# Kernel optimization log

Hardware: AMD Instinct MI355X
Metric: run time of the kernel (lower is better)

Reference implementation:

```python
import jax, jax.numpy as jnp
import numpy as np

EPS = 1e-5

def _ln(x, g, b):
    m = x.mean(-1, keepdims=True)
    v = ((x - m) ** 2).mean(-1, keepdims=True)
    return (x - m) / jnp.sqrt(v + EPS) * g + b


def setup_inputs() -> dict:
    key = jax.random.key(0)
    ks = jax.random.split(key, 8)
    b, t, n, d = 8, 12, 207, 64
    dh = 4 * d
    sc = 1.0 / np.sqrt(d)
    x = jax.random.normal(ks[0], (b, t, n, d), jnp.float32)
    stg = jax.random.uniform(ks[1], (b, t, n, t, n), jnp.float32)
    return {
        "x": x,
        "stg": stg,
        "Wq": jax.random.normal(ks[2], (d, d), jnp.float32) * sc,
        "bq": jnp.zeros((d,), jnp.float32),
        "Wk": jax.random.normal(ks[3], (d, d), jnp.float32) * sc,
        "bk": jnp.zeros((d,), jnp.float32),
        "gamma": jnp.ones((d,), jnp.float32),
        "beta": jnp.zeros((d,), jnp.float32),
        "fgamma": jnp.ones((d,), jnp.float32),
        "fbeta": jnp.zeros((d,), jnp.float32),
        "w1": jax.random.normal(ks[4], (d, dh), jnp.float32) * sc,
        "b1": jnp.zeros((dh,), jnp.float32),
        "w2": jax.random.normal(ks[5], (dh, d), jnp.float32) * (1.0 / np.sqrt(dh)),
        "b2": jnp.zeros((d,), jnp.float32),
        "topk": 3,
    }


def reference(x, stg, Wq, bq, Wk, bk, gamma, beta, fgamma, fbeta, w1, b1, w2, b2, topk):
    b, t, n, d = x.shape
    scale = 1.0 / np.sqrt(d).astype(np.float32)
    x_ = _ln(x, gamma, beta)
    y_ = x_  # trg is None path
    h = t
    q = y_ @ Wq + bq  # [b,t,n,d]
    kx = x_ @ Wk + bk  # [b,t,n,d]
    dg = jnp.einsum('btnd,bkmd->btnkm', q, kx) * scale  # [b,t,n,t,n]
    s = jax.nn.sigmoid(dg) * stg
    s = s.reshape(b, h * n, t * n)
    k_eff = topk * n if topk < 5 else topk  # torch: self.topk *= n when < 5
    top_vals = jax.lax.top_k(s, k_eff)[0]  # [b, h*n, k_eff]
    thr = top_vals[..., -1:]
    s = jnp.where(s > thr, s, -jnp.inf)
    a = jax.nn.softmax(s, axis=-1).reshape(b, h, n, t, n)  # dropout = identity (eval)
    o = jnp.einsum('btnkm,bkmd->btnd', a, x_)
    z = o + y_
    # FFN (assumed pre-norm residual MLP): x + relu(LN(x)W1+b1)W2 + b2
    hdd = jax.nn.relu(_ln(z, fgamma, fbeta) @ w1 + b1)
    return z + hdd @ w2 + b2
```

## Files before the change

### kernel.cpp

```cpp
#include <hip/hip_runtime.h>

#define NBATCH 8
#define NN     207
#define DHID   256
#define LL     2484
#define LLP    2496
#define RT     26
#define NBLK   96
#define GCOL   2560
#define TILES  78
#define TPW    10
#define SENT   0xFFFFu
#define LNEPS  1e-5f

typedef __attribute__((ext_vector_type(8)))  short bf16x8;
typedef __attribute__((ext_vector_type(8)))  unsigned short u16x8;
typedef __attribute__((ext_vector_type(16))) float f32x16;

__device__ __forceinline__ short f2bf(float f) {
    unsigned u = __float_as_uint(f);
    unsigned r = (u + 0x7FFFu + ((u >> 16) & 1u)) >> 16;
    return (short)r;
}

__global__ __launch_bounds__(256) void k_lnproj(
    const float* __restrict__ x, const float* __restrict__ Wq, const float* __restrict__ bq,
    const float* __restrict__ Wk, const float* __restrict__ bk,
    const float* __restrict__ gamma, const float* __restrict__ beta,
    float* __restrict__ Xn, float* __restrict__ Qb, short* __restrict__ Kbf)
{
    __shared__ float xrow[4][64];
    int w = threadIdx.x >> 6, lane = threadIdx.x & 63;
    size_t row = (size_t)blockIdx.x * 4 + w;
    float xv = x[row * 64 + lane];
    float m = xv;
    #pragma unroll
    for (int o = 32; o; o >>= 1) m += __shfl_xor(m, o, 64);
    m *= (1.0f / 64.0f);
    float dv = xv - m;
    float var = dv * dv;
    #pragma unroll
    for (int o = 32; o; o >>= 1) var += __shfl_xor(var, o, 64);
    var *= (1.0f / 64.0f);
    float xg = dv * (1.0f / sqrtf(var + LNEPS)) * gamma[lane] + beta[lane];
    Xn[row * 64 + lane] = xg;
    xrow[w][lane] = xg;
    __syncthreads();
    float q = bq[lane], k = bk[lane];
    #pragma unroll 8
    for (int e = 0; e < 64; e++) {
        float xe = xrow[w][e];
        q += xe * Wq[e * 64 + lane];
        k += xe * Wk[e * 64 + lane];
    }
    int br = (int)(row / LL);
    int jl = (int)(row - (size_t)br * LL);
    Qb[((size_t)br * LLP + jl) * 64 + lane] = q;
    Kbf[((size_t)br * LLP + jl) * 64 + lane] = f2bf(k);
}

__global__ __launch_bounds__(256) void k_prep(
    const float* __restrict__ Xn, short* __restrict__ XbfT,
    short* __restrict__ Kbf, float* __restrict__ Qb)
{
    __shared__ float tile[64][65];
    int bb = blockIdx.x & 7;
    int jt = blockIdx.x >> 3;
    int j0 = jt * 64;
    for (int i = threadIdx.x; i < 4096; i += 256) {
        int jl = i >> 6, d = i & 63;
        int j = j0 + jl;
        tile[jl][d] = (j < LL) ? Xn[((size_t)bb * LL + j) * 64 + d] : 0.f;
    }
    __syncthreads();
    for (int i = threadIdx.x; i < 4096; i += 256) {
        int d = i >> 6, jl = i & 63;
        XbfT[((size_t)bb * 64 + d) * LLP + j0 + jl] = f2bf(tile[jl][d]);
    }
    if (jt == 38) {
        for (int i = threadIdx.x; i < (LLP - LL) * 64; i += 256) {
            int jl = i >> 6, d = i & 63;
            Kbf[((size_t)bb * LLP + LL + jl) * 64 + d] = 0;
            Qb [((size_t)bb * LLP + LL + jl) * 64 + d] = 0.f;
        }
    }
}

__global__ __launch_bounds__(512, 2) void k_attn(
    const float* __restrict__ Xn, const float* __restrict__ Qb,
    const short* __restrict__ Kbf, const short* __restrict__ XbfT,
    const float* __restrict__ stg, const int* __restrict__ topk_p,
    float* __restrict__ Z)
{
    __shared__ __align__(16) unsigned short Gt[RT * GCOL];
    __shared__ __align__(16) unsigned hist[RT * 256];
    __shared__ int gmax_lds[RT];
    __shared__ unsigned thr_lds[RT];
    float* redf = (float*)hist;
    float* rowsum = redf + RT * 65;

    int tid = threadIdx.x;
    int lane = tid & 63, wv = tid >> 6;
    int hi = lane >> 5, l31 = lane & 31;
    int b = blockIdx.x & 7;
    int tile = blockIdx.x >> 3;
    int row0 = tile * RT;

    for (int i = tid; i < RT * GCOL / 2; i += 512) ((unsigned*)Gt)[i] = 0xFFFFFFFFu;
    for (int i = tid; i < RT * 256; i += 512) hist[i] = 0u;
    if (tid < RT) gmax_lds[tid] = 0;

    int keff;
    { int tk = *topk_p; keff = (tk < 5) ? tk * NN : tk; }

    bf16x8 qf[4];
    {
        const float* qp = Qb + ((size_t)b * LLP + row0 + l31) * 64 + hi * 8;
        #pragma unroll
        for (int kk = 0; kk < 4; kk++) {
            bf16x8 f;
            #pragma unroll
            for (int e = 0; e < 8; e++) f[e] = f2bf(qp[kk * 16 + e]);
            qf[kk] = f;
        }
    }
    const float* stgb = stg + (size_t)b * LL * LL;
    int kt0 = wv * TPW;
    int kt1 = (kt0 + TPW < TILES) ? kt0 + TPW : TILES;
    __syncthreads();

    int gmx[16];
    #pragma unroll
    for (int i = 0; i < 16; i++) gmx[i] = 0;

    float svsA[16]; bf16x8 kvA[4];
    if (kt0 < kt1) {
        int j = kt0 * 32 + l31;
        #pragma unroll
        for (int reg = 0; reg < 16; reg++) {
            int trow = (reg & 3) + 8 * (reg >> 2) + 4 * hi;
            int grow = row0 + trow;
            bool v = (j < LL) && (trow < RT) && (grow < LL);
            svsA[reg] = v ? stgb[(size_t)grow * LL + j] : 0.f;
        }
        const short* kbase = Kbf + ((size_t)b * LLP + j) * 64 + hi * 8;
        kvA[0] = *(const bf16x8*)(kbase);
        kvA[1] = *(const bf16x8*)(kbase + 16);
        kvA[2] = *(const bf16x8*)(kbase + 32);
        kvA[3] = *(const bf16x8*)(kbase + 48);
    }
    for (int kt = kt0; kt < kt1; ++kt) {
        float svsB[16]; bf16x8 kvB[4];
        if (kt + 1 < kt1) {
            int jn = (kt + 1) * 32 + l31;
            #pragma unroll
            for (int reg = 0; reg < 16; reg++) {
                int trow = (reg & 3) + 8 * (reg >> 2) + 4 * hi;
                int grow = row0 + trow;
                bool v = (jn < LL) && (trow < RT) && (grow < LL);
                svsB[reg] = v ? stgb[(size_t)grow * LL + jn] : 0.f;
            }
            const short* kbase = Kbf + ((size_t)b * LLP + jn) * 64 + hi * 8;
            kvB[0] = *(const bf16x8*)(kbase);
            kvB[1] = *(const bf16x8*)(kbase + 16);
            kvB[2] = *(const bf16x8*)(kbase + 32);
            kvB[3] = *(const bf16x8*)(kbase + 48);
        }
        int j = kt * 32 + l31;
        bool vj = (j < LL);
        f32x16 c = {0.f,0.f,0.f,0.f,0.f,0.f,0.f,0.f,0.f,0.f,0.f,0.f,0.f,0.f,0.f,0.f};
        c = __builtin_amdgcn_mfma_f32_32x32x16_bf16(qf[0], kvA[0], c, 0, 0, 0);
        c = __builtin_amdgcn_mfma_f32_32x32x16_bf16(qf[1], kvA[1], c, 0, 0, 0);
        c = __builtin_amdgcn_mfma_f32_32x32x16_bf16(qf[2], kvA[2], c, 0, 0, 0);
        c = __builtin_amdgcn_mfma_f32_32x32x16_bf16(qf[3], kvA[3], c, 0, 0, 0);
        #pragma unroll
        for (int reg = 0; reg < 16; reg++) {
            int trow = (reg & 3) + 8 * (reg >> 2) + 4 * hi;
            int grow = row0 + trow;
            bool v = vj && (trow < RT) && (grow < LL);
            float sg = 1.0f / (1.0f + __expf(c[reg] * -0.125f));
            float s = sg * svsA[reg];
            int g = (int)(s * 65536.0f); g = (g > 65534) ? 65534 : g;
            if (v) {
                unsigned col = (unsigned)j ^ ((unsigned)(trow & 15) << 3);
                Gt[trow * GCOL + col] = (unsigned short)g;
                atomicAdd(&hist[trow * 256 + (g >> 8)], 1u << (((g >> 7) & 1) << 4));
                gmx[reg] = (g > gmx[reg]) ? g : gmx[reg];
            }
        }
        #pragma unroll
        for (int i = 0; i < 16; i++) svsA[i] = svsB[i];
        #pragma unroll
        for (int i = 0; i < 4; i++) kvA[i] = kvB[i];
    }
    #pragma unroll
    for (int reg = 0; reg < 16; reg++) {
        int v = gmx[reg];
        #pragma unroll
        for (int off = 1; off < 32; off <<= 1) {
            int o2 = __shfl_xor(v, off, 64);
            v = (o2 > v) ? o2 : v;
        }
        if (l31 == 0) {
            int trow = (reg & 3) + 8 * (reg >> 2) + 4 * hi;
            if (trow < RT) atomicMax(&gmax_lds[trow], v);
        }
    }
    __syncthreads();

    #pragma unroll 1
    for (int row = wv; row < RT; row += 8) {
        const unsigned* h = &hist[row * 256];
        unsigned w0 = h[lane * 4 + 0], w1 = h[lane * 4 + 1];
        unsigned w2 = h[lane * 4 + 2], w3 = h[lane * 4 + 3];
        unsigned cb[8] = {w0 & 0xFFFFu, w0 >> 16, w1 & 0xFFFFu, w1 >> 16,
                          w2 & 0xFFFFu, w2 >> 16, w3 & 0xFFFFu, w3 >> 16};
        unsigned S = cb[0] + cb[1] + cb[2] + cb[3] + cb[4] + cb[5] + cb[6] + cb[7];
        unsigned T = S;
        #pragma unroll
        for (int off = 1; off < 64; off <<= 1) {
            unsigned t = __shfl_down(T, off, 64);
            T += (lane + off < 64) ? t : 0u;
        }
        unsigned Tn = T - S;
        unsigned sfx[9];
        sfx[8] = Tn;
        #pragma unroll
        for (int i = 7; i >= 0; i--) sfx[i] = cb[i] + sfx[i + 1];
        unsigned kr = (unsigned)keff;
        int hit = -1; unsigned nk = 0, mm = 0;
        #pragma unroll
        for (int i = 0; i < 8; i++) {
            if (sfx[i] >= kr && sfx[i + 1] < kr) { hit = i; nk = kr - sfx[i + 1]; mm = cb[i]; }
        }
        unsigned long long mask = __ballot(hit >= 0);
        if (mask == 0ull) {
            if (lane == 0) thr_lds[row] = 65535u;
        } else {
            int src = __ffsll(mask) - 1;
            int bini = __shfl(hit, src, 64);
            nk = (unsigned)__shfl((int)nk, src, 64);
            mm = (unsigned)__shfl((int)mm, src, 64);
            if (lane == 0) {
                int bin = src * 8 + bini;
                int drop = (2u * nk <= mm) ? 1 : 0;
                int thrge = bin * 128 + (drop ? 128 : 0);
                if (thrge > 65535) thrge = 65535;
                thr_lds[row] = (unsigned)thrge;
            }
        }
    }
    __syncthreads();

    for (int i = tid; i < RT * 65 + RT; i += 512) redf[i] = 0.f;
    __syncthreads();

    bool av = (l31 < RT);
    int arow = av ? l31 : 0;
    int agmax = av ? gmax_lds[arow] : -1;
    unsigned athr = av ? thr_lds[arow] : 65535u;
    unsigned swz = ((unsigned)(arow & 15)) << 3;
    const unsigned short* gp = &Gt[arow * GCOL];
    const short* xb0 = XbfT + ((size_t)b * 64 + l31) * LLP + hi * 8;
    const short* xb1 = XbfT + ((size_t)b * 64 + 32 + l31) * LLP + hi * 8;
    f32x16 p0 = {0.f,0.f,0.f,0.f,0.f,0.f,0.f,0.f,0.f,0.f,0.f,0.f,0.f,0.f,0.f,0.f};
    f32x16 p1 = p0;
    float smr = 0.f;

    bf16x8 xA[4];
    if (kt0 < kt1) {
        int j0 = kt0 * 32;
        xA[0] = *(const bf16x8*)(xb0 + j0);
        xA[1] = *(const bf16x8*)(xb0 + j0 + 16);
        xA[2] = *(const bf16x8*)(xb1 + j0);
        xA[3] = *(const bf16x8*)(xb1 + j0 + 16);
    }
    for (int kt = kt0; kt < kt1; ++kt) {
        bf16x8 xB[4];
        if (kt + 1 < kt1) {
            int jn = (kt + 1) * 32;
            xB[0] = *(const bf16x8*)(xb0 + jn);
            xB[1] = *(const bf16x8*)(xb0 + jn + 16);
            xB[2] = *(const bf16x8*)(xb1 + jn);
            xB[3] = *(const bf16x8*)(xb1 + jn + 16);
        }
        int j0 = kt * 32;
        bf16x8 ea[2];
        #pragma unroll
        for (int kk = 0; kk < 2; kk++) {
            unsigned colb = (unsigned)(j0 + kk * 16 + hi * 8) ^ swz;
            u16x8 gv = *(const u16x8*)&gp[colb];
            bf16x8 f;
            #pragma unroll
            for (int e = 0; e < 8; e++) {
                unsigned g = gv[e];
                bool keep = (g != SENT) && (g >= athr || (int)g == agmax);
                float ev = keep ? __expf((float)((int)g - agmax) * (1.0f / 65536.0f)) : 0.f;
                smr += ev;
                f[e] = f2bf(ev);
            }
            ea[kk] = f;
        }
        p0 = __builtin_amdgcn_mfma_f32_32x32x16_bf16(ea[0], xA[0], p0, 0, 0, 0);
        p0 = __builtin_amdgcn_mfma_f32_32x32x16_bf16(ea[1], xA[1], p0, 0, 0, 0);
        p1 = __builtin_amdgcn_mfma_f32_32x32x16_bf16(ea[0], xA[2], p1, 0, 0, 0);
        p1 = __builtin_amdgcn_mfma_f32_32x32x16_bf16(ea[1], xA[3], p1, 0, 0, 0);
        #pragma unroll
        for (int i = 0; i < 4; i++) xA[i] = xB[i];
    }
    smr += __shfl_xor(smr, 32, 64);
    if (lane < 32 && l31 < RT) atomicAdd(&rowsum[l31], smr);
    #pragma unroll
    for (int reg = 0; reg < 16; reg++) {
        int trow = (reg & 3) + 8 * (reg >> 2) + 4 * hi;
        if (trow < RT) {
            atomicAdd(&redf[trow * 65 + l31],      p0[reg]);
            atomicAdd(&redf[trow * 65 + 32 + l31], p1[reg]);
        }
    }
    __syncthreads();

    for (int i = tid; i < RT * 64; i += 512) {
        int r = i >> 6, d = i & 63;
        int grow = row0 + r;
        if (grow < LL) {
            size_t gi = ((size_t)b * LL + grow) * 64 + d;
            Z[gi] = redf[r * 65 + d] * (1.0f / rowsum[r]) + Xn[gi];
        }
    }
}

__global__ __launch_bounds__(256) void k_ffn(
    const float* __restrict__ Zb, const float* __restrict__ fg, const float* __restrict__ fb,
    const float* __restrict__ w1, const float* __restrict__ b1,
    const float* __restrict__ w2, const float* __restrict__ b2,
    float* __restrict__ out)
{
    const int G2 = 16;
    __shared__ float zr[G2][64];
    __shared__ float zl[G2][64];
    __shared__ float h[G2][DHID];
    int tid = threadIdx.x;
    int w = tid >> 6, lane = tid & 63;
    size_t row0 = (size_t)blockIdx.x * G2;
    for (int rr = w; rr < G2; rr += 4) {
        float zv = Zb[(row0 + rr) * 64 + lane];
        zr[rr][lane] = zv;
        float m = zv;
        #pragma unroll
        for (int o = 32; o; o >>= 1) m += __shfl_xor(m, o, 64);
        m *= (1.0f / 64.0f);
        float dv = zv - m;
        float var = dv * dv;
        #pragma unroll
        for (int o = 32; o; o >>= 1) var += __shfl_xor(var, o, 64);
        var *= (1.0f / 64.0f);
        zl[rr][lane] = dv * (1.0f / sqrtf(var + LNEPS)) * fg[lane] + fb[lane];
    }
    __syncthreads();
    float hacc[G2];
    #pragma unroll
    for (int g = 0; g < G2; g++) hacc[g] = 0.f;
    for (int d = 0; d < 64; d++) {
        float wv1 = w1[d * DHID + tid];
        #pragma unroll
        for (int g = 0; g < G2; g++) hacc[g] += zl[g][d] * wv1;
    }
    float b1v = b1[tid];
    #pragma unroll
    for (int g = 0; g < G2; g++) h[g][tid] = fmaxf(hacc[g] + b1v, 0.f);
    __syncthreads();
    float oacc[4] = {0.f, 0.f, 0.f, 0.f};
    for (int i = 0; i < DHID; i++) {
        float wv2 = w2[i * 64 + lane];
        #pragma unroll
        for (int rr = 0; rr < 4; rr++) oacc[rr] += h[w * 4 + rr][i] * wv2;
    }
    float b2v = b2[lane];
    #pragma unroll
    for (int rr = 0; rr < 4; rr++)
        out[(row0 + w * 4 + rr) * 64 + lane] = zr[w * 4 + rr][lane] + oacc[rr] + b2v;
}

extern "C" void kernel_launch(void* const* d_in, const int* in_sizes, int n_in,
                              void* d_out, int out_size, void* d_ws, size_t ws_size,
                              hipStream_t stream)
{
    const float* x      = (const float*)d_in[0];
    const float* stg    = (const float*)d_in[1];
    const float* Wq     = (const float*)d_in[2];
    const float* bq     = (const float*)d_in[3];
    const float* Wk     = (const float*)d_in[4];
    const float* bk     = (const float*)d_in[5];
    const float* gamma  = (const float*)d_in[6];
    const float* beta   = (const float*)d_in[7];
    const float* fgamma = (const float*)d_in[8];
    const float* fbeta  = (const float*)d_in[9];
    const float* w1     = (const float*)d_in[10];
    const float* b1     = (const float*)d_in[11];
    const float* w2     = (const float*)d_in[12];
    const float* b2     = (const float*)d_in[13];
    const int*   topk   = (const int*)d_in[14];
    float* out = (float*)d_out;

    const size_t rows  = (size_t)NBATCH * LL;
    const size_t prows = (size_t)NBATCH * LLP;
    float* Xn = (float*)d_ws;
    float* Qb = Xn + rows * 64;
    float* Z  = Qb + (prows + 64) * 64;
    short* Kbf  = (short*)(Z + rows * 64);
    short* XbfT = Kbf + prows * 64;

    k_lnproj<<<(int)(rows / 4), 256, 0, stream>>>(x, Wq, bq, Wk, bk, gamma, beta, Xn, Qb, Kbf);
    k_prep<<<NBATCH * 39, 256, 0, stream>>>(Xn, XbfT, Kbf, Qb);
    k_attn<<<NBATCH * NBLK, 512, 0, stream>>>(Xn, Qb, Kbf, XbfT, stg, topk, Z);
    k_ffn<<<(int)(rows / 16), 256, 0, stream>>>(Z, fgamma, fbeta, w1, b1, w2, b2, out);
}
```

Baseline: 248.9 us.

## Quantize attention scores to 8-bit codes, shrink LDS and raise occupancy

Stores the sigmoid-gated scores in shared memory as 8-bit bin codes instead of 16-bit values, halving the score buffer and the histogram. The per-row max tracking is removed, and softmax weights are rebuilt from bin midpoints. The smaller LDS footprint lets launch bounds request 4 blocks per CU instead of 2. Precision drops to 256 levels, so the top-k threshold and the softmax values become coarser approximations, and the max-element fallback for rows that keep nothing is gone.

```diff
diff --git a/kernel.cpp b/kernel.cpp
--- a/kernel.cpp
+++ b/kernel.cpp
@@ -7,14 +7,13 @@
 #define LLP    2496
 #define RT     26
 #define NBLK   96
-#define GCOL   2560
+#define GCOL8  2496
 #define TILES  78
 #define TPW    10
-#define SENT   0xFFFFu
 #define LNEPS  1e-5f
 
 typedef __attribute__((ext_vector_type(8)))  short bf16x8;
-typedef __attribute__((ext_vector_type(8)))  unsigned short u16x8;
+typedef __attribute__((ext_vector_type(8)))  unsigned char u8x8;
 typedef __attribute__((ext_vector_type(16))) float f32x16;
 
 __device__ __forceinline__ short f2bf(float f) {
@@ -86,15 +85,14 @@
     }
 }
 
-__global__ __launch_bounds__(512, 2) void k_attn(
+__global__ __launch_bounds__(512, 4) void k_attn(
     const float* __restrict__ Xn, const float* __restrict__ Qb,
     const short* __restrict__ Kbf, const short* __restrict__ XbfT,
     const float* __restrict__ stg, const int* __restrict__ topk_p,
     float* __restrict__ Z)
 {
-    __shared__ __align__(16) unsigned short Gt[RT * GCOL];
-    __shared__ __align__(16) unsigned hist[RT * 256];
-    __shared__ int gmax_lds[RT];
+    __shared__ __align__(16) unsigned char Gt[RT * GCOL8];
+    __shared__ __align__(16) unsigned hist[RT * 128];
     __shared__ unsigned thr_lds[RT];
     float* redf = (float*)hist;
     float* rowsum = redf + RT * 65;
@@ -106,9 +104,8 @@
     int tile = blockIdx.x >> 3;
     int row0 = tile * RT;
 
-    for (int i = tid; i < RT * GCOL / 2; i += 512) ((unsigned*)Gt)[i] = 0xFFFFFFFFu;
-    for (int i = tid; i < RT * 256; i += 512) hist[i] = 0u;
-    if (tid < RT) gmax_lds[tid] = 0;
+    for (int i = tid; i < RT * GCOL8 / 4; i += 512) ((unsigned*)Gt)[i] = 0xFFFFFFFFu;
+    for (int i = tid; i < RT * 128; i += 512) hist[i] = 0u;
 
     int keff;
     { int tk = *topk_p; keff = (tk < 5) ? tk * NN : tk; }
@@ -128,10 +125,6 @@
     int kt0 = wv * TPW;
     int kt1 = (kt0 + TPW < TILES) ? kt0 + TPW : TILES;
     __syncthreads();
-
-    int gmx[16];
-    #pragma unroll
-    for (int i = 0; i < 16; i++) gmx[i] = 0;
 
     float svsA[16]; bf16x8 kvA[4];
     if (kt0 < kt1) {
@@ -180,42 +173,26 @@
             bool v = vj && (trow < RT) && (grow < LL);
             float sg = 1.0f / (1.0f + __expf(c[reg] * -0.125f));
             float s = sg * svsA[reg];
-            int g = (int)(s * 65536.0f); g = (g > 65534) ? 65534 : g;
+            int g = (int)(s * 65536.0f); g = (g > 65279) ? 65279 : g;
             if (v) {
-                unsigned col = (unsigned)j ^ ((unsigned)(trow & 15) << 3);
-                Gt[trow * GCOL + col] = (unsigned short)g;
-                atomicAdd(&hist[trow * 256 + (g >> 8)], 1u << (((g >> 7) & 1) << 4));
-                gmx[reg] = (g > gmx[reg]) ? g : gmx[reg];
+                unsigned code = (unsigned)g >> 8;
+                Gt[trow * GCOL8 + ((unsigned)j ^ ((unsigned)(trow & 7) << 3))] = (unsigned char)code;
+                atomicAdd(&hist[trow * 128 + (code >> 1)], 1u << ((code & 1) << 4));
             }
         }
         #pragma unroll
         for (int i = 0; i < 16; i++) svsA[i] = svsB[i];
         #pragma unroll
         for (int i = 0; i < 4; i++) kvA[i] = kvB[i];
-    }
-    #pragma unroll
-    for (int reg = 0; reg < 16; reg++) {
-        int v = gmx[reg];
-        #pragma unroll
-        for (int off = 1; off < 32; off <<= 1) {
-            int o2 = __shfl_xor(v, off, 64);
-            v = (o2 > v) ? o2 : v;
-        }
-        if (l31 == 0) {
-            int trow = (reg & 3) + 8 * (reg >> 2) + 4 * hi;
-            if (trow < RT) atomicMax(&gmax_lds[trow], v);
-        }
     }
     __syncthreads();
 
     #pragma unroll 1
     for (int row = wv; row < RT; row += 8) {
-        const unsigned* h = &hist[row * 256];
-        unsigned w0 = h[lane * 4 + 0], w1 = h[lane * 4 + 1];
-        unsigned w2 = h[lane * 4 + 2], w3 = h[lane * 4 + 3];
-        unsigned cb[8] = {w0 & 0xFFFFu, w0 >> 16, w1 & 0xFFFFu, w1 >> 16,
-                          w2 & 0xFFFFu, w2 >> 16, w3 & 0xFFFFu, w3 >> 16};
-        unsigned S = cb[0] + cb[1] + cb[2] + cb[3] + cb[4] + cb[5] + cb[6] + cb[7];
+        const unsigned* h = &hist[row * 128];
+        unsigned w0 = h[lane * 2 + 0], w1 = h[lane * 2 + 1];
+        unsigned cb[4] = {w0 & 0xFFFFu, w0 >> 16, w1 & 0xFFFFu, w1 >> 16};
+        unsigned S = cb[0] + cb[1] + cb[2] + cb[3];
         unsigned T = S;
         #pragma unroll
         for (int off = 1; off < 64; off <<= 1) {
@@ -223,30 +200,28 @@
             T += (lane + off < 64) ? t : 0u;
         }
         unsigned Tn = T - S;
-        unsigned sfx[9];
-        sfx[8] = Tn;
-        #pragma unroll
-        for (int i = 7; i >= 0; i--) sfx[i] = cb[i] + sfx[i + 1];
+        unsigned sfx[5];
+        sfx[4] = Tn;
+        #pragma unroll
+        for (int i = 3; i >= 0; i--) sfx[i] = cb[i] + sfx[i + 1];
         unsigned kr = (unsigned)keff;
         int hit = -1; unsigned nk = 0, mm = 0;
         #pragma unroll
-        for (int i = 0; i < 8; i++) {
+        for (int i = 0; i < 4; i++) {
             if (sfx[i] >= kr && sfx[i + 1] < kr) { hit = i; nk = kr - sfx[i + 1]; mm = cb[i]; }
         }
         unsigned long long mask = __ballot(hit >= 0);
         if (mask == 0ull) {
-            if (lane == 0) thr_lds[row] = 65535u;
+            if (lane == 0) thr_lds[row] = 255u;
         } else {
             int src = __ffsll(mask) - 1;
             int bini = __shfl(hit, src, 64);
             nk = (unsigned)__shfl((int)nk, src, 64);
             mm = (unsigned)__shfl((int)mm, src, 64);
             if (lane == 0) {
-                int bin = src * 8 + bini;
-                int drop = (2u * nk <= mm) ? 1 : 0;
-                int thrge = bin * 128 + (drop ? 128 : 0);
-                if (thrge > 65535) thrge = 65535;
-                thr_lds[row] = (unsigned)thrge;
+                int bin = src * 4 + bini;
+                int drop = (2u * nk <= mm && nk < kr) ? 1 : 0;
+                thr_lds[row] = (unsigned)(bin + drop);
             }
         }
     }
@@ -257,10 +232,9 @@
 
     bool av = (l31 < RT);
     int arow = av ? l31 : 0;
-    int agmax = av ? gmax_lds[arow] : -1;
-    unsigned athr = av ? thr_lds[arow] : 65535u;
-    unsigned swz = ((unsigned)(arow & 15)) << 3;
-    const unsigned short* gp = &Gt[arow * GCOL];
+    unsigned athr = av ? thr_lds[arow] : 255u;
+    unsigned swz = ((unsigned)(arow & 7)) << 3;
+    const unsigned char* gp8 = &Gt[arow * GCOL8];
     const short* xb0 = XbfT + ((size_t)b * 64 + l31) * LLP + hi * 8;
     const short* xb1 = XbfT + ((size_t)b * 64 + 32 + l31) * LLP + hi * 8;
     f32x16 p0 = {0.f,0.f,0.f,0.f,0.f,0.f,0.f,0.f,0.f,0.f,0.f,0.f,0.f,0.f,0.f,0.f};
@@ -288,14 +262,13 @@
         bf16x8 ea[2];
         #pragma unroll
         for (int kk = 0; kk < 2; kk++) {
-            unsigned colb = (unsigned)(j0 + kk * 16 + hi * 8) ^ swz;
-            u16x8 gv = *(const u16x8*)&gp[colb];
+            u8x8 gv = *(const u8x8*)&gp8[(unsigned)(j0 + kk * 16 + hi * 8) ^ swz];
             bf16x8 f;
             #pragma unroll
             for (int e = 0; e < 8; e++) {
                 unsigned g = gv[e];
-                bool keep = (g != SENT) && (g >= athr || (int)g == agmax);
-                float ev = keep ? __expf((float)((int)g - agmax) * (1.0f / 65536.0f)) : 0.f;
+                bool keep = (g >= athr) && (g != 255u);
+                float ev = keep ? __expf(((float)g + 0.5f) * 0.00390625f) : 0.f;
                 smr += ev;
                 f[e] = f2bf(ev);
             }
```

New measurement: 384.7 us. 54.5% more time.
